# Optimization experiments

Hardware: AMD Instinct MI355X
Metric: run time of the kernel (lower is better)

## Reference

```python
import jax, jax.numpy as jnp
import numpy as np

B, L, D = 2, 2048, 1024
NUM_HEADS = 16
HEAD_DIM = D // NUM_HEADS


def setup_inputs() -> dict:
    key = jax.random.key(0)
    k1, k2 = jax.random.split(key)
    x = jax.random.normal(k1, (B, L, D), dtype=jnp.float32)
    # torch Linear(input_dim, 3*output_dim, bias=False); store as [in, 3*out] for x @ W
    W_qkv = jax.random.normal(k2, (D, 3 * D), dtype=jnp.float32) * (1.0 / np.sqrt(D))
    return {"x": x, "W_qkv": W_qkv}


def reference(x, W_qkv):
    b, l, d = x.shape
    h, hd = NUM_HEADS, HEAD_DIM
    qkv = x @ W_qkv                                  # [B, L, 3*D]
    qkv = qkv.reshape(b, l, 3, h, hd)
    q = jnp.transpose(qkv[:, :, 0], (0, 2, 1, 3))    # [B, H, L, hd]
    k = jnp.transpose(qkv[:, :, 1], (0, 2, 1, 3))
    v = jnp.transpose(qkv[:, :, 2], (0, 2, 1, 3))
    scale = 1.0 / jnp.sqrt(jnp.asarray(hd, dtype=x.dtype))
    scores = jnp.einsum('bhqd,bhkd->bhqk', q, k) * scale   # [B, H, L, L]
    causal = jnp.triu(jnp.ones((l, l), dtype=bool), k=1)   # True above diagonal -> masked
    scores = jnp.where(causal, -jnp.inf, scores)
    attn = jax.nn.softmax(scores, axis=-1)
    # dropout p=0.0 -> identity (eval mode)
    out = jnp.einsum('bhqk,bhkd->bhqd', attn, v)            # [B, H, L, hd]
    out = jnp.transpose(out, (0, 2, 1, 3)).reshape(b, l, h * hd)
    return out
```

## Files before the change

kernel.cpp:

```cpp
#include <hip/hip_runtime.h>
#include <hip/hip_bf16.h>
#include <math.h>

#define NB_L 2048
#define GM 4096
#define GN 3072
#define GK 1024
#define NROWS 65536
#define SCALE_L2E 0.180336880f

typedef float  f4v __attribute__((ext_vector_type(4)));
typedef short  s4v __attribute__((ext_vector_type(4)));
typedef short  s8v __attribute__((ext_vector_type(8)));

#define MFMA_16x16x32(a, b, c) __builtin_amdgcn_mfma_f32_16x16x32_bf16((a), (b), (c), 0, 0, 0)
#define MFMA_16x16x16(a, b, c) __builtin_amdgcn_mfma_f32_16x16x16bf16_1k((a), (b), (c), 0, 0, 0)

static __device__ __forceinline__ unsigned int bfpk(float a, float b) {
    __hip_bfloat162 h = __float22bfloat162_rn(float2{a, b});
    union { __hip_bfloat162 h2; unsigned int u; } cv; cv.h2 = h; return cv.u;
}
static __device__ __forceinline__ unsigned short bf1(float a) {
    union { __hip_bfloat16 h; unsigned short u; } cv; cv.h = __float2bfloat16(a); return cv.u;
}
static __device__ __forceinline__ float bf2f(unsigned short u) {
    union { unsigned int u; float f; } cv; cv.u = ((unsigned int)u) << 16; return cv.f;
}

static __device__ __forceinline__ void gl_lds16(const ushort* g, ushort* l) {
    __builtin_amdgcn_global_load_lds((const __attribute__((address_space(1))) void*)g,
                                     (__attribute__((address_space(3))) void*)l, 16, 0, 0);
}

__global__ __launch_bounds__(256) void conv_fused(
    const float* __restrict__ X, const float* __restrict__ W,
    ushort* __restrict__ Xb, ushort* __restrict__ Wt)
{
    __shared__ __align__(16) ushort T[64][72];
    const int bid = blockIdx.x, t = threadIdx.x;
    if (bid < 2048) {
        const int i = bid * 256 + t;
        const float4 f0 = ((const float4*)X)[2 * i];
        const float4 f1 = ((const float4*)X)[2 * i + 1];
        uint4 u;
        u.x = bfpk(f0.x, f0.y); u.y = bfpk(f0.z, f0.w);
        u.z = bfpk(f1.x, f1.y); u.w = bfpk(f1.z, f1.w);
        ((uint4*)Xb)[i] = u;
    } else {
        const int wb = bid - 2048;
        const int k0 = (wb & 15) * 64, n0 = (wb >> 4) * 64;
        {
            const int kr = t >> 2, nc0 = (t & 3) * 16;
            const float* src = W + (size_t)(k0 + kr) * GN + n0 + nc0;
#pragma unroll
            for (int u = 0; u < 4; ++u) {
                const float4 v = *(const float4*)(src + 4 * u);
                T[nc0 + 4 * u + 0][kr] = bf1(v.x);
                T[nc0 + 4 * u + 1][kr] = bf1(v.y);
                T[nc0 + 4 * u + 2][kr] = bf1(v.z);
                T[nc0 + 4 * u + 3][kr] = bf1(v.w);
            }
        }
        __syncthreads();
        {
            const int nr = t >> 2, kc0 = (t & 3) * 16;
            ushort* dst = Wt + (size_t)(n0 + nr) * GK + k0 + kc0;
            *(s8v*)dst       = *(const s8v*)&T[nr][kc0];
            *(s8v*)(dst + 8) = *(const s8v*)&T[nr][kc0 + 8];
        }
    }
}

__global__ __launch_bounds__(512, 2) void qkv_gemm_bf16(
    const ushort* __restrict__ Xb, const ushort* __restrict__ Wt,
    ushort* __restrict__ Qh, ushort* __restrict__ Kh, ushort* __restrict__ VT)
{
    __shared__ __align__(16) ushort As[2][2][256][32];
    __shared__ __align__(16) ushort Bs[2][2][256][32];

    const int tid = threadIdx.x;
    const int bid = blockIdx.x;

    const int xcd = bid & 7, idx = bid >> 3;
    const int ytile = ((xcd >> 1) << 2) + (idx & 3);
    const int xtile = (xcd & 1) * 6 + (idx >> 2);
    const int row0 = ytile << 8, col0 = xtile << 8;

    const int lane = tid & 63, w = tid >> 6;
    const int wm = w >> 2, wn = w & 3;
    const int lq = lane & 15, quad = lane >> 4;

    const int rA = tid >> 2, pA = tid & 3;
    const int cA = pA ^ ((rA >> 1) & 3);
    const ushort* gA0 = Xb + (size_t)(row0 + rA) * GK + cA * 8;
    const ushort* gB0 = Wt + (size_t)(col0 + rA) * GK + cA * 8;

    const int pq = (quad ^ ((lq >> 1) & 3)) * 8;
    const int rowA = wm * 128 + lq;
    const int rowB = wn * 64 + lq;

    f4v acc[8][4];
#pragma unroll
    for (int mf = 0; mf < 8; ++mf)
#pragma unroll
        for (int nf = 0; nf < 4; ++nf) acc[mf][nf] = 0.f;

    auto stA = [&](int t, int h, int u) {
        gl_lds16(gA0 + (size_t)u * 128 * GK + t * 64 + h * 32,
                 &As[t & 1][h][u * 128 + rA][pA * 8]);
    };
    auto stB = [&](int t, int h, int u) {
        gl_lds16(gB0 + (size_t)u * 128 * GK + t * 64 + h * 32,
                 &Bs[t & 1][h][u * 128 + rA][pA * 8]);
    };

    stA(0, 0, 0); stA(0, 0, 1);
    stB(0, 0, 0); stB(0, 0, 1);
    stB(0, 1, 0); stB(0, 1, 1);
    stA(0, 1, 0); stA(0, 1, 1);
    stA(1, 0, 0); stA(1, 0, 1);
    stB(1, 0, 0); stB(1, 0, 1);
    asm volatile("s_waitcnt vmcnt(4)" ::: "memory");
    __builtin_amdgcn_s_barrier();
    asm volatile("" ::: "memory");

    const int NT = GK / 64;
#pragma unroll 2
    for (int t = 0; t < NT; ++t) {
        const int cur = t & 1;
        s8v af[4], bfr[4];

#pragma unroll
        for (int nf = 0; nf < 4; ++nf) bfr[nf] = *(const s8v*)&Bs[cur][0][rowB + nf * 16][pq];
#pragma unroll
        for (int mf = 0; mf < 4; ++mf) af[mf] = *(const s8v*)&As[cur][0][rowA + mf * 16][pq];
        if (t + 1 < NT) { stB(t + 1, 1, 0); stB(t + 1, 1, 1); }
        __builtin_amdgcn_s_barrier();
        asm volatile("s_waitcnt lgkmcnt(0)");
        __builtin_amdgcn_s_setprio(1);
#pragma unroll
        for (int mf = 0; mf < 4; ++mf)
#pragma unroll
            for (int nf = 0; nf < 4; ++nf)
                acc[mf][nf] = MFMA_16x16x32(af[mf], bfr[nf], acc[mf][nf]);
        __builtin_amdgcn_s_setprio(0);
        __builtin_amdgcn_s_barrier();

#pragma unroll
        for (int mf = 0; mf < 4; ++mf) af[mf] = *(const s8v*)&As[cur][0][rowA + 64 + mf * 16][pq];
        if (t + 1 < NT) { stA(t + 1, 1, 0); stA(t + 1, 1, 1); }
        __builtin_amdgcn_s_barrier();
        asm volatile("s_waitcnt lgkmcnt(0)");
        __builtin_amdgcn_s_setprio(1);
#pragma unroll
        for (int mf = 0; mf < 4; ++mf)
#pragma unroll
            for (int nf = 0; nf < 4; ++nf)
                acc[mf + 4][nf] = MFMA_16x16x32(af[mf], bfr[nf], acc[mf + 4][nf]);
        __builtin_amdgcn_s_setprio(0);
        __builtin_amdgcn_s_barrier();

#pragma unroll
        for (int nf = 0; nf < 4; ++nf) bfr[nf] = *(const s8v*)&Bs[cur][1][rowB + nf * 16][pq];
#pragma unroll
        for (int mf = 0; mf < 4; ++mf) af[mf] = *(const s8v*)&As[cur][1][rowA + mf * 16][pq];
        if (t + 2 < NT) { stA(t + 2, 0, 0); stA(t + 2, 0, 1); }
        __builtin_amdgcn_s_barrier();
        asm volatile("s_waitcnt lgkmcnt(0)");
        __builtin_amdgcn_s_setprio(1);
#pragma unroll
        for (int mf = 0; mf < 4; ++mf)
#pragma unroll
            for (int nf = 0; nf < 4; ++nf)
                acc[mf][nf] = MFMA_16x16x32(af[mf], bfr[nf], acc[mf][nf]);
        __builtin_amdgcn_s_setprio(0);
        __builtin_amdgcn_s_barrier();

#pragma unroll
        for (int mf = 0; mf < 4; ++mf) af[mf] = *(const s8v*)&As[cur][1][rowA + 64 + mf * 16][pq];
        if (t + 2 < NT) { stB(t + 2, 0, 0); stB(t + 2, 0, 1); }
        __builtin_amdgcn_s_barrier();
        asm volatile("s_waitcnt lgkmcnt(0)");
        __builtin_amdgcn_s_setprio(1);
#pragma unroll
        for (int mf = 0; mf < 4; ++mf)
#pragma unroll
            for (int nf = 0; nf < 4; ++nf)
                acc[mf + 4][nf] = MFMA_16x16x32(af[mf], bfr[nf], acc[mf + 4][nf]);
        __builtin_amdgcn_s_setprio(0);
        if (t + 2 < NT) asm volatile("s_waitcnt vmcnt(4)" ::: "memory");
        else            asm volatile("s_waitcnt vmcnt(0)" ::: "memory");
        __builtin_amdgcn_s_barrier();
        asm volatile("" ::: "memory");
    }

    const int part = xtile >> 2;
#pragma unroll
    for (int mf = 0; mf < 8; ++mf)
#pragma unroll
        for (int nf = 0; nf < 4; ++nf) {
            const int colp = (col0 & 1023) + wn * 64 + nf * 16 + lq;
            const int hh = colp >> 6, d = colp & 63;
#pragma unroll
            for (int r = 0; r < 4; ++r) {
                const int row = row0 + wm * 128 + mf * 16 + quad * 4 + r;
                const int b = row >> 11, tok = row & 2047;
                const int bh = b * 16 + hh;
                if (part == 0) {
                    Qh[((size_t)bh * 2048 + tok) * 64 + d] = bf1(acc[mf][nf][r] * SCALE_L2E);
                } else if (part == 1) {
                    Kh[((size_t)bh * 2048 + tok) * 64 + (d ^ ((tok & 7) << 3))] = bf1(acc[mf][nf][r]);
                } else {
                    VT[((size_t)bh * 64 + d) * 2048 + (tok ^ ((d & 7) << 3))] = bf1(acc[mf][nf][r]);
                }
            }
        }
}

__global__ __launch_bounds__(256, 4) void attn_bf16(
    const ushort* __restrict__ Qh, const ushort* __restrict__ Kh,
    const ushort* __restrict__ VT, ushort* __restrict__ Opart, float* __restrict__ Lp)
{
    __shared__ __align__(16) ushort Ks[2][64 * 64];
    __shared__ __align__(16) ushort Vt[2][64 * 64];

    const int x = blockIdx.x;
    const int bh = x & 31;
    const int qlow = (x >> 5) & 7;
    const int s = (x >> 8) & 1;
    const int x9 = (x >> 9) & 1;
    const int qt = x9 ? (15 - qlow) : qlow;

    const int tid = threadIdx.x;
    const int w = tid >> 6, lane = tid & 63;
    const int lq = lane & 15, quad = lane >> 4;
    const int kswz = (lq & 7) << 3;
    const int qrow_base = qt * 128 + w * 32;
    const int diag = 2 * qt + (w >> 1);

    s8v qf[2][2];
#pragma unroll
    for (int qg = 0; qg < 2; ++qg)
#pragma unroll
        for (int sb = 0; sb < 2; ++sb)
            qf[qg][sb] = *(const s8v*)(Qh + ((size_t)bh * 2048 + qrow_base + qg * 16 + lq) * 64
                                       + sb * 32 + quad * 8);

    f4v o[4][2];
#pragma unroll
    for (int dg = 0; dg < 4; ++dg)
#pragma unroll
        for (int qg = 0; qg < 2; ++qg) o[dg][qg] = 0.f;
    f4v lacc[2]; lacc[0] = 0.f; lacc[1] = 0.f;
    const s4v ones = { (short)0x3F80, (short)0x3F80, (short)0x3F80, (short)0x3F80 };

    const int kt_lo = s ? (qt + 1) : 0;
    const int kt_hi = s ? (2 * qt + 1) : qt;
    const int niter = kt_hi - kt_lo + 1;

    const ushort* kbase = Kh + (size_t)bh * 2048 * 64;
    const ushort* vbase = VT + (size_t)bh * 64 * 2048;
    const int g1 = tid, g2 = tid + 256;
    const int kr1 = g1 >> 3, ko1 = (g1 & 7) * 8;
    const int kr2 = g2 >> 3, ko2 = (g2 & 7) * 8;

    auto stage = [&](int kt, int bufi) {
        const ushort* kt_k = kbase + (size_t)kt * 64 * 64;
        const ushort* kt_v = vbase + kt * 64;
        gl_lds16(kt_k + kr1 * 64 + ko1,           &Ks[bufi][g1 * 8]);
        gl_lds16(kt_k + kr2 * 64 + ko2,           &Ks[bufi][g2 * 8]);
        gl_lds16(kt_v + (size_t)kr1 * 2048 + ko1, &Vt[bufi][g1 * 8]);
        gl_lds16(kt_v + (size_t)kr2 * 2048 + ko2, &Vt[bufi][g2 * 8]);
    };

    auto compute = [&](int ktc, int bufi) {
        if (ktc > diag) return;
        f4v st[4][2];
#pragma unroll
        for (int kg = 0; kg < 4; ++kg)
#pragma unroll
            for (int qg = 0; qg < 2; ++qg) st[kg][qg] = 0.f;
#pragma unroll
        for (int kg = 0; kg < 4; ++kg)
#pragma unroll
            for (int sb = 0; sb < 2; ++sb) {
                const s8v af = *(const s8v*)&Ks[bufi][(kg * 16 + lq) * 64
                                                     + ((sb * 32 + quad * 8) ^ kswz)];
#pragma unroll
                for (int qg = 0; qg < 2; ++qg)
                    st[kg][qg] = MFMA_16x16x32(af, qf[qg][sb], st[kg][qg]);
            }
        if (ktc == diag) {
#pragma unroll
            for (int kg = 0; kg < 4; ++kg)
#pragma unroll
                for (int qg = 0; qg < 2; ++qg) {
                    const int qrow = qrow_base + qg * 16 + lq;
#pragma unroll
                    for (int r = 0; r < 4; ++r)
                        if (ktc * 64 + kg * 16 + quad * 4 + r > qrow)
                            st[kg][qg][r] = -INFINITY;
                }
        }
#pragma unroll
        for (int kg = 0; kg < 4; ++kg)
#pragma unroll
            for (int qg = 0; qg < 2; ++qg)
#pragma unroll
                for (int r = 0; r < 4; ++r)
                    st[kg][qg][r] = exp2f(st[kg][qg][r]);
#pragma unroll
        for (int ks = 0; ks < 4; ++ks) {
            s4v pb[2];
#pragma unroll
            for (int qg = 0; qg < 2; ++qg) {
                union { s4v v; uint2 u; } c;
                c.u.x = bfpk(st[ks][qg][0], st[ks][qg][1]);
                c.u.y = bfpk(st[ks][qg][2], st[ks][qg][3]);
                pb[qg] = c.v;
            }
#pragma unroll
            for (int qg = 0; qg < 2; ++qg)
                lacc[qg] = MFMA_16x16x16(ones, pb[qg], lacc[qg]);
#pragma unroll
            for (int dg = 0; dg < 4; ++dg) {
                const s4v va = *(const s4v*)&Vt[bufi][(dg * 16 + lq) * 64
                                                     + ((ks * 16 + quad * 4) ^ kswz)];
#pragma unroll
                for (int qg = 0; qg < 2; ++qg)
                    o[dg][qg] = MFMA_16x16x16(va, pb[qg], o[dg][qg]);
            }
        }
    };

    stage(kt_lo, 0);
    for (int i = 0; i < niter; ++i) {
        const int cur = i & 1;
        __syncthreads();
        if (i + 1 < niter) stage(kt_lo + i + 1, cur ^ 1);
        compute(kt_lo + i, cur);
    }

#pragma unroll
    for (int qg = 0; qg < 2; ++qg) {
        const size_t prow = (size_t)(s * 32 + bh) * 2048 + qrow_base + qg * 16 + lq;
#pragma unroll
        for (int dg = 0; dg < 4; ++dg) {
            const int d = dg * 16 + quad * 4;
            uint2 u;
            u.x = bfpk(o[dg][qg][0], o[dg][qg][1]);
            u.y = bfpk(o[dg][qg][2], o[dg][qg][3]);
            *(uint2*)&Opart[prow * 64 + d] = u;
        }
        if (quad == 0) Lp[prow] = lacc[qg][0];
    }
}

__global__ __launch_bounds__(256) void attn_combine(
    const ushort* __restrict__ Opart, const float* __restrict__ Lp, float* __restrict__ Out)
{
    const int id = blockIdx.x * 256 + threadIdx.x;
    const int row = id >> 4, c4 = (id & 15) * 4;
    const float l0 = Lp[row], l1 = Lp[row + NROWS];
    const float inv = 1.0f / (l0 + l1);

    const s4v a = *(const s4v*)&Opart[(size_t)row * 64 + c4];
    const s4v c = *(const s4v*)&Opart[(size_t)(row + NROWS) * 64 + c4];
    float4 v;
    v.x = (bf2f((unsigned short)a[0]) + bf2f((unsigned short)c[0])) * inv;
    v.y = (bf2f((unsigned short)a[1]) + bf2f((unsigned short)c[1])) * inv;
    v.z = (bf2f((unsigned short)a[2]) + bf2f((unsigned short)c[2])) * inv;
    v.w = (bf2f((unsigned short)a[3]) + bf2f((unsigned short)c[3])) * inv;

    const int bh = row >> 11, qrow = row & 2047;
    const int b = bh >> 4, h = bh & 15;
    *(float4*)(Out + ((size_t)(b * 2048 + qrow)) * 1024 + h * 64 + c4) = v;
}

extern "C" void kernel_launch(void* const* d_in, const int* in_sizes, int n_in,
                              void* d_out, int out_size, void* d_ws, size_t ws_size,
                              hipStream_t stream)
{
    const float* x  = (const float*)d_in[0];
    const float* wq = (const float*)d_in[1];
    float* out = (float*)d_out;

    const size_t HEADTEN = (size_t)32 * 2048 * 64;
    ushort* wsp = (ushort*)d_ws;
    ushort* qh = wsp;
    ushort* kh = qh + HEADTEN;
    ushort* vt = kh + HEADTEN;
    ushort* xb = vt + HEADTEN;
    ushort* wt = xb + (size_t)GM * GK;
    ushort* opart = xb;
    float*  lp    = (float*)(opart + (size_t)2 * NROWS * 64);

    conv_fused<<<2816, 256, 0, stream>>>(x, wq, xb, wt);
    qkv_gemm_bf16<<<192, 512, 0, stream>>>(xb, wt, qh, kh, vt);
    attn_bf16<<<1024, 256, 0, stream>>>(qh, kh, vt, opart, lp);
    attn_combine<<<NROWS * 16 / 256, 256, 0, stream>>>(opart, lp, out);
}
```

Before: 177.6 us.

## Retile QKV GEMM to 128x192 blocks with 256 threads for better CU fill

Changes the QKV projection GEMM from 192 blocks of 256x256 tiles with 512 threads to 512 blocks of 128x192 tiles with 256 threads. Each of the four waves now covers all 128 rows and a 48-column slice, and the epilogue works out the Q/K/V part per column because a tile can now span two parts. The goal is to fill all 256 CUs with more blocks and reduce the tail imbalance left by 192 blocks. In exchange each tile reuses its loads less, so global and LDS traffic per flop goes up.

```diff
diff --git a/kernel.cpp b/kernel.cpp
--- a/kernel.cpp
+++ b/kernel.cpp
@@ -71,56 +71,55 @@
     }
 }
 
-__global__ __launch_bounds__(512, 2) void qkv_gemm_bf16(
+__global__ __launch_bounds__(256, 2) void qkv_gemm_bf16(
     const ushort* __restrict__ Xb, const ushort* __restrict__ Wt,
     ushort* __restrict__ Qh, ushort* __restrict__ Kh, ushort* __restrict__ VT)
 {
-    __shared__ __align__(16) ushort As[2][2][256][32];
-    __shared__ __align__(16) ushort Bs[2][2][256][32];
+    __shared__ __align__(16) ushort As[2][2][128][32];
+    __shared__ __align__(16) ushort Bs[2][2][192][32];
 
     const int tid = threadIdx.x;
     const int bid = blockIdx.x;
 
     const int xcd = bid & 7, idx = bid >> 3;
-    const int ytile = ((xcd >> 1) << 2) + (idx & 3);
-    const int xtile = (xcd & 1) * 6 + (idx >> 2);
-    const int row0 = ytile << 8, col0 = xtile << 8;
-
-    const int lane = tid & 63, w = tid >> 6;
-    const int wm = w >> 2, wn = w & 3;
+    const int ytile = ((xcd >> 1) << 3) + (idx & 7);
+    const int xtile = ((xcd & 1) << 3) + (idx >> 3);
+    const int row0 = ytile << 7;
+    const int col0 = xtile * 192;
+
+    const int lane = tid & 63, wn = tid >> 6;
     const int lq = lane & 15, quad = lane >> 4;
 
-    const int rA = tid >> 2, pA = tid & 3;
-    const int cA = pA ^ ((rA >> 1) & 3);
-    const ushort* gA0 = Xb + (size_t)(row0 + rA) * GK + cA * 8;
-    const ushort* gB0 = Wt + (size_t)(col0 + rA) * GK + cA * 8;
+    const int rS = tid >> 2, pA = tid & 3;
+    const int cA = pA ^ ((rS >> 1) & 3);
+    const ushort* gA0 = Xb + (size_t)(row0 + rS) * GK + cA * 8;
+    const ushort* gB0 = Wt + (size_t)(col0 + rS) * GK + cA * 8;
 
     const int pq = (quad ^ ((lq >> 1) & 3)) * 8;
-    const int rowA = wm * 128 + lq;
-    const int rowB = wn * 64 + lq;
-
-    f4v acc[8][4];
+    const int rowB = wn * 48;
+
+    f4v acc[8][3];
 #pragma unroll
     for (int mf = 0; mf < 8; ++mf)
 #pragma unroll
-        for (int nf = 0; nf < 4; ++nf) acc[mf][nf] = 0.f;
+        for (int nf = 0; nf < 3; ++nf) acc[mf][nf] = 0.f;
 
     auto stA = [&](int t, int h, int u) {
-        gl_lds16(gA0 + (size_t)u * 128 * GK + t * 64 + h * 32,
-                 &As[t & 1][h][u * 128 + rA][pA * 8]);
+        gl_lds16(gA0 + (size_t)u * 64 * GK + t * 64 + h * 32,
+                 &As[t & 1][h][u * 64 + rS][pA * 8]);
     };
     auto stB = [&](int t, int h, int u) {
-        gl_lds16(gB0 + (size_t)u * 128 * GK + t * 64 + h * 32,
-                 &Bs[t & 1][h][u * 128 + rA][pA * 8]);
+        gl_lds16(gB0 + (size_t)u * 64 * GK + t * 64 + h * 32,
+                 &Bs[t & 1][h][u * 64 + rS][pA * 8]);
     };
 
     stA(0, 0, 0); stA(0, 0, 1);
-    stB(0, 0, 0); stB(0, 0, 1);
-    stB(0, 1, 0); stB(0, 1, 1);
+    stB(0, 0, 0); stB(0, 0, 1); stB(0, 0, 2);
     stA(0, 1, 0); stA(0, 1, 1);
+    stB(0, 1, 0); stB(0, 1, 1); stB(0, 1, 2);
     stA(1, 0, 0); stA(1, 0, 1);
-    stB(1, 0, 0); stB(1, 0, 1);
-    asm volatile("s_waitcnt vmcnt(4)" ::: "memory");
+    stB(1, 0, 0); stB(1, 0, 1); stB(1, 0, 2);
+    asm volatile("s_waitcnt vmcnt(5)" ::: "memory");
     __builtin_amdgcn_s_barrier();
     asm volatile("" ::: "memory");
 
@@ -128,26 +127,26 @@
 #pragma unroll 2
     for (int t = 0; t < NT; ++t) {
         const int cur = t & 1;
-        s8v af[4], bfr[4];
-
-#pragma unroll
-        for (int nf = 0; nf < 4; ++nf) bfr[nf] = *(const s8v*)&Bs[cur][0][rowB + nf * 16][pq];
-#pragma unroll
-        for (int mf = 0; mf < 4; ++mf) af[mf] = *(const s8v*)&As[cur][0][rowA + mf * 16][pq];
-        if (t + 1 < NT) { stB(t + 1, 1, 0); stB(t + 1, 1, 1); }
+        s8v af[4], bfr[3];
+
+#pragma unroll
+        for (int nf = 0; nf < 3; ++nf) bfr[nf] = *(const s8v*)&Bs[cur][0][rowB + nf * 16 + lq][pq];
+#pragma unroll
+        for (int mf = 0; mf < 4; ++mf) af[mf] = *(const s8v*)&As[cur][0][mf * 16 + lq][pq];
+        if (t + 1 < NT) { stB(t + 1, 1, 0); stB(t + 1, 1, 1); stB(t + 1, 1, 2); }
         __builtin_amdgcn_s_barrier();
         asm volatile("s_waitcnt lgkmcnt(0)");
         __builtin_amdgcn_s_setprio(1);
 #pragma unroll
         for (int mf = 0; mf < 4; ++mf)
 #pragma unroll
-            for (int nf = 0; nf < 4; ++nf)
+            for (int nf = 0; nf < 3; ++nf)
                 acc[mf][nf] = MFMA_16x16x32(af[mf], bfr[nf], acc[mf][nf]);
         __builtin_amdgcn_s_setprio(0);
         __builtin_amdgcn_s_barrier();
 
 #pragma unroll
-        for (int mf = 0; mf < 4; ++mf) af[mf] = *(const s8v*)&As[cur][0][rowA + 64 + mf * 16][pq];
+        for (int mf = 0; mf < 4; ++mf) af[mf] = *(const s8v*)&As[cur][0][64 + mf * 16 + lq][pq];
         if (t + 1 < NT) { stA(t + 1, 1, 0); stA(t + 1, 1, 1); }
         __builtin_amdgcn_s_barrier();
         asm volatile("s_waitcnt lgkmcnt(0)");
@@ -155,15 +154,15 @@
 #pragma unroll
         for (int mf = 0; mf < 4; ++mf)
 #pragma unroll
-            for (int nf = 0; nf < 4; ++nf)
+            for (int nf = 0; nf < 3; ++nf)
                 acc[mf + 4][nf] = MFMA_16x16x32(af[mf], bfr[nf], acc[mf + 4][nf]);
         __builtin_amdgcn_s_setprio(0);
         __builtin_amdgcn_s_barrier();
 
 #pragma unroll
-        for (int nf = 0; nf < 4; ++nf) bfr[nf] = *(const s8v*)&Bs[cur][1][rowB + nf * 16][pq];
-#pragma unroll
-        for (int mf = 0; mf < 4; ++mf) af[mf] = *(const s8v*)&As[cur][1][rowA + mf * 16][pq];
+        for (int nf = 0; nf < 3; ++nf) bfr[nf] = *(const s8v*)&Bs[cur][1][rowB + nf * 16 + lq][pq];
+#pragma unroll
+        for (int mf = 0; mf < 4; ++mf) af[mf] = *(const s8v*)&As[cur][1][mf * 16 + lq][pq];
         if (t + 2 < NT) { stA(t + 2, 0, 0); stA(t + 2, 0, 1); }
         __builtin_amdgcn_s_barrier();
         asm volatile("s_waitcnt lgkmcnt(0)");
@@ -171,39 +170,40 @@
 #pragma unroll
         for (int mf = 0; mf < 4; ++mf)
 #pragma unroll
-            for (int nf = 0; nf < 4; ++nf)
+            for (int nf = 0; nf < 3; ++nf)
                 acc[mf][nf] = MFMA_16x16x32(af[mf], bfr[nf], acc[mf][nf]);
         __builtin_amdgcn_s_setprio(0);
         __builtin_amdgcn_s_barrier();
 
 #pragma unroll
-        for (int mf = 0; mf < 4; ++mf) af[mf] = *(const s8v*)&As[cur][1][rowA + 64 + mf * 16][pq];
-        if (t + 2 < NT) { stB(t + 2, 0, 0); stB(t + 2, 0, 1); }
+        for (int mf = 0; mf < 4; ++mf) af[mf] = *(const s8v*)&As[cur][1][64 + mf * 16 + lq][pq];
+        if (t + 2 < NT) { stB(t + 2, 0, 0); stB(t + 2, 0, 1); stB(t + 2, 0, 2); }
         __builtin_amdgcn_s_barrier();
         asm volatile("s_waitcnt lgkmcnt(0)");
         __builtin_amdgcn_s_setprio(1);
 #pragma unroll
         for (int mf = 0; mf < 4; ++mf)
 #pragma unroll
-            for (int nf = 0; nf < 4; ++nf)
+            for (int nf = 0; nf < 3; ++nf)
                 acc[mf + 4][nf] = MFMA_16x16x32(af[mf], bfr[nf], acc[mf + 4][nf]);
         __builtin_amdgcn_s_setprio(0);
-        if (t + 2 < NT) asm volatile("s_waitcnt vmcnt(4)" ::: "memory");
+        if (t + 2 < NT) asm volatile("s_waitcnt vmcnt(5)" ::: "memory");
         else            asm volatile("s_waitcnt vmcnt(0)" ::: "memory");
         __builtin_amdgcn_s_barrier();
         asm volatile("" ::: "memory");
     }
 
-    const int part = xtile >> 2;
 #pragma unroll
     for (int mf = 0; mf < 8; ++mf)
 #pragma unroll
-        for (int nf = 0; nf < 4; ++nf) {
-            const int colp = (col0 & 1023) + wn * 64 + nf * 16 + lq;
+        for (int nf = 0; nf < 3; ++nf) {
+            const int colg = col0 + wn * 48 + nf * 16 + lq;
+            const int part = colg >> 10;
+            const int colp = colg & 1023;
             const int hh = colp >> 6, d = colp & 63;
 #pragma unroll
             for (int r = 0; r < 4; ++r) {
-                const int row = row0 + wm * 128 + mf * 16 + quad * 4 + r;
+                const int row = row0 + mf * 16 + quad * 4 + r;
                 const int b = row >> 11, tok = row & 2047;
                 const int bh = b * 16 + hh;
                 if (part == 0) {
@@ -396,7 +396,7 @@
     float*  lp    = (float*)(opart + (size_t)2 * NROWS * 64);
 
     conv_fused<<<2816, 256, 0, stream>>>(x, wq, xb, wt);
-    qkv_gemm_bf16<<<192, 512, 0, stream>>>(xb, wt, qh, kh, vt);
+    qkv_gemm_bf16<<<512, 256, 0, stream>>>(xb, wt, qh, kh, vt);
     attn_bf16<<<1024, 256, 0, stream>>>(qh, kh, vt, opart, lp);
     attn_combine<<<NROWS * 16 / 256, 256, 0, stream>>>(opart, lp, out);
 }
```

Measured after the change: 171.3 us. 1.04x faster.
